# Optimization experiments

Measured on AMD Instinct MI355X. Metric: run time of the kernel, lower is better.

Reference implementation:

```python
import jax, jax.numpy as jnp
import numpy as np


def setup_inputs() -> dict:
    key = jax.random.key(0)
    k0, k1, k2 = jax.random.split(key, 3)
    B, S, H, D = 2, 2048, 16, 128  # flash-attn layout [batch, seq, heads, head_dim]
    q = jax.random.normal(k0, (B, S, H, D), dtype=jnp.float32)
    k = jax.random.normal(k1, (B, S, H, D), dtype=jnp.float32)
    v = jax.random.normal(k2, (B, S, H, D), dtype=jnp.float32)
    return {"_in0": q, "_in1": k, "_in2": v}


def reference(_in0, _in1, _in2):
    # Ring attention computes exact (non-causal, default) scaled dot-product
    # attention over the full sequence; the ring KV rotation is a distributed
    # execution detail, not a change in math. Single-device math:
    q, k, v = _in0, _in1, _in2
    D = q.shape[-1]
    scale = 1.0 / jnp.sqrt(jnp.asarray(D, dtype=q.dtype))
    # scores: [B, H, Sq, Sk]
    scores = jnp.einsum("bqhd,bkhd->bhqk", q, k) * scale
    probs = jax.nn.softmax(scores, axis=-1)
    out = jnp.einsum("bhqk,bkhd->bqhd", probs, v)
    return out
```

## Files before the change

### kernel.cpp

```cpp
#include <hip/hip_runtime.h>
#include <hip/hip_bf16.h>

typedef __attribute__((ext_vector_type(8))) short short8;
typedef __attribute__((ext_vector_type(16))) float f32x16;
typedef __attribute__((ext_vector_type(4))) unsigned int uint4v;

#define NB 2
#define NS 2048
#define NH 16
#define ND 128
#define ROWS (NH * ND)
#define KVBLK 64
#define QBLK 128
#define NTILE (NS / KVBLK)
#define NQB (NS / QBLK)

__device__ __forceinline__ unsigned short f2bf(float f) {
  union { __hip_bfloat16 b; unsigned short u; } c;
  c.b = __float2bfloat16(f);
  return c.u;
}

__device__ __forceinline__ short8 pack8(float4 a, float4 b, float s) {
  short8 r;
  r[0] = (short)f2bf(a.x * s); r[1] = (short)f2bf(a.y * s);
  r[2] = (short)f2bf(a.z * s); r[3] = (short)f2bf(a.w * s);
  r[4] = (short)f2bf(b.x * s); r[5] = (short)f2bf(b.y * s);
  r[6] = (short)f2bf(b.z * s); r[7] = (short)f2bf(b.w * s);
  return r;
}

__device__ __forceinline__ void dma16(const void* g, void* l) {
  __builtin_amdgcn_global_load_lds(
      (const __attribute__((address_space(1))) unsigned int*)g,
      (__attribute__((address_space(3))) unsigned int*)l, 16, 0, 0);
}

__device__ __forceinline__ void pl32swap(unsigned int& a, unsigned int& b) {
  asm("v_permlane32_swap_b32 %0, %1" : "+v"(a), "+v"(b));
}

__global__ __launch_bounds__(256) void prepass_kv(
    const float* __restrict__ Kg, const float* __restrict__ Vg,
    unsigned short* __restrict__ Kb, unsigned short* __restrict__ Vt) {
  const int blk = blockIdx.x;
  const int t = blk & (NTILE - 1);
  const int bh = blk >> 5;
  const int h = bh & (NH - 1);
  const int b = bh >> 4;
  const int tid = threadIdx.x;

  const size_t ibase = (size_t)b * NS * ROWS + (size_t)h * ND + (size_t)t * KVBLK * ROWS;
  const float* Kp = Kg + ibase;
  const float* Vp = Vg + ibase;
  unsigned short* Kbp = Kb + ((size_t)bh * NS + t * KVBLK) * ND;
  unsigned short* Vtp = Vt + (size_t)bh * ND * NS + t * KVBLK;

#pragma unroll
  for (int j = 0; j < 4; ++j) {
    const int r = j * 16 + (tid >> 4);
    const int c0 = (tid & 15) * 8;
    float4 a = *reinterpret_cast<const float4*>(Kp + (size_t)r * ROWS + c0);
    float4 c = *reinterpret_cast<const float4*>(Kp + (size_t)r * ROWS + c0 + 4);
    *reinterpret_cast<short8*>(Kbp + r * ND + c0) = pack8(a, c, 1.0f);
  }

  __shared__ float vt[64][129];
#pragma unroll
  for (int j = 0; j < 4; ++j) {
    const int r = j * 16 + (tid >> 4);
    const int c0 = (tid & 15) * 8;
    float4 a = *reinterpret_cast<const float4*>(Vp + (size_t)r * ROWS + c0);
    float4 c = *reinterpret_cast<const float4*>(Vp + (size_t)r * ROWS + c0 + 4);
    vt[r][c0 + 0] = a.x; vt[r][c0 + 1] = a.y; vt[r][c0 + 2] = a.z; vt[r][c0 + 3] = a.w;
    vt[r][c0 + 4] = c.x; vt[r][c0 + 5] = c.y; vt[r][c0 + 6] = c.z; vt[r][c0 + 7] = c.w;
  }
  __syncthreads();
#pragma unroll
  for (int dj = 0; dj < 4; ++dj) {
    const int d = dj * 32 + (tid >> 3);
    const int s0 = (tid & 7) * 8;
    short8 o8;
#pragma unroll
    for (int k = 0; k < 8; ++k) o8[k] = (short)f2bf(vt[s0 + k][d]);
    *reinterpret_cast<short8*>(Vtp + (size_t)d * NS + s0) = o8;
  }
}

__global__ __launch_bounds__(256, 2) void fattn_fwd(
    const float* __restrict__ Qg, const unsigned short* __restrict__ Kb,
    const unsigned short* __restrict__ Vt, float* __restrict__ Og) {
  __shared__ __align__(16) char lds[65536];
  const int tid = threadIdx.x;
  const int l = tid & 63;
  const int w = tid >> 6;
  const int l31 = l & 31;
  const int hi2 = l >> 5;

  const int orig = blockIdx.x;
  const int wg = (orig & 7) * 64 + (orig >> 3);
  const int qblk = wg & (NQB - 1);
  const int bh = wg >> 4;
  const int h = bh & (NH - 1);
  const int b = bh >> 4;

  const float* Qp = Qg + (size_t)b * NS * ROWS + (size_t)h * ND;
  float* Op = Og + (size_t)b * NS * ROWS + (size_t)h * ND;
  const char* Kbh = (const char*)(Kb + (size_t)bh * NS * ND);
  const char* Vth = (const char*)(Vt + (size_t)bh * ND * NS);

  const float scale = 0.08838834764831845f * 1.4426950408889634f;

  const int qrow = qblk * QBLK + w * 32 + l31;
  short8 qf[8];
  {
    const float* qr = Qp + (size_t)qrow * ROWS + hi2 * 8;
#pragma unroll
    for (int ks = 0; ks < 8; ++ks) {
      float4 a = *reinterpret_cast<const float4*>(qr + ks * 16);
      float4 c = *reinterpret_cast<const float4*>(qr + ks * 16 + 4);
      qf[ks] = pack8(a, c, scale);
    }
  }

  auto stage = [&](int t, char* kd, char* vd) {
    const char* Kt = Kbh + (size_t)t * KVBLK * 256;
#pragma unroll
    for (int i = 0; i < 4; ++i) {
      const int instr = w * 4 + i;
      const int row = instr * 4 + (l >> 4);
      const int x = (l & 15) << 4;
      dma16(Kt + row * 256 + (x ^ ((row & 7) << 4)), kd + instr * 1024);
    }
    const char* Vtt = Vth + (size_t)t * KVBLK * 2;
#pragma unroll
    for (int j = 0; j < 4; ++j) {
      const int instr = w * 4 + j;
      const int d = instr * 8 + (l >> 3);
      const int x = (l & 7) << 4;
      dma16(Vtt + (size_t)d * (NS * 2) + (x ^ ((d & 7) << 4)), vd + instr * 1024);
    }
  };

  f32x16 o[4];
#pragma unroll
  for (int dt = 0; dt < 4; ++dt) o[dt] = 0.f;
  float l_acc = 0.f;

  stage(0, lds, lds + 16384);
  asm volatile("s_waitcnt vmcnt(0)" ::: "memory");
  __syncthreads();

#pragma unroll 1
  for (int t = 0; t < NTILE; ++t) {
    char* ksb = lds + (t & 1) * 32768;
    char* vtb = ksb + 16384;
    if (t + 1 < NTILE) {
      char* kn = lds + ((t + 1) & 1) * 32768;
      stage(t + 1, kn, kn + 16384);
    }

    f32x16 st[2];
    __builtin_amdgcn_s_setprio(1);
#pragma unroll
    for (int mt = 0; mt < 2; ++mt) {
      f32x16 acc = 0.f;
      const int row = mt * 32 + l31;
#pragma unroll
      for (int ks = 0; ks < 8; ++ks) {
        short8 kf = *reinterpret_cast<const short8*>(
            ksb + row * 256 + ((ks * 32 + hi2 * 16) ^ ((row & 7) << 4)));
        acc = __builtin_amdgcn_mfma_f32_32x32x16_bf16(kf, qf[ks], acc, 0, 0, 0);
      }
      st[mt] = acc;
    }
    __builtin_amdgcn_s_setprio(0);

    f32x16 p0, p1;
#pragma unroll
    for (int r = 0; r < 16; ++r) p0[r] = exp2f(st[0][r]);
#pragma unroll
    for (int r = 0; r < 16; ++r) p1[r] = exp2f(st[1][r]);
    {
      float s = 0.f;
#pragma unroll
      for (int r = 0; r < 16; ++r) s += p0[r] + p1[r];
      l_acc += s;
    }

    short8 pf[4];
#pragma unroll
    for (int mt = 0; mt < 2; ++mt) {
      const f32x16& pp = mt ? p1 : p0;
      unsigned int X[8];
#pragma unroll
      for (int j = 0; j < 8; ++j)
        X[j] = (unsigned int)f2bf(pp[2 * j]) | ((unsigned int)f2bf(pp[2 * j + 1]) << 16);
      pl32swap(X[0], X[2]); pl32swap(X[1], X[3]);
      pl32swap(X[4], X[6]); pl32swap(X[5], X[7]);
      uint4v lo_ = {X[0], X[1], X[2], X[3]};
      uint4v hi_ = {X[4], X[5], X[6], X[7]};
      pf[mt * 2 + 0] = __builtin_bit_cast(short8, lo_);
      pf[mt * 2 + 1] = __builtin_bit_cast(short8, hi_);
    }

    __builtin_amdgcn_s_setprio(1);
#pragma unroll
    for (int dt = 0; dt < 4; ++dt) {
      const int d = dt * 32 + l31;
#pragma unroll
      for (int ks = 0; ks < 4; ++ks) {
        short8 vf = *reinterpret_cast<const short8*>(
            vtb + d * 128 + ((ks * 32 + hi2 * 16) ^ ((d & 7) << 4)));
        o[dt] = __builtin_amdgcn_mfma_f32_32x32x16_bf16(vf, pf[ks], o[dt], 0, 0, 0);
      }
    }
    __builtin_amdgcn_s_setprio(0);

    if (t + 1 < NTILE) {
      asm volatile("s_waitcnt vmcnt(0)" ::: "memory");
      __syncthreads();
    }
  }

  const float lt = l_acc + __shfl_xor(l_acc, 32);
  const float inv = 1.0f / lt;
  float* orow = Op + (size_t)qrow * ROWS;
#pragma unroll
  for (int dt = 0; dt < 4; ++dt) {
#pragma unroll
    for (int g = 0; g < 4; ++g) {
      float4 v;
      v.x = o[dt][g * 4 + 0] * inv;
      v.y = o[dt][g * 4 + 1] * inv;
      v.z = o[dt][g * 4 + 2] * inv;
      v.w = o[dt][g * 4 + 3] * inv;
      *reinterpret_cast<float4*>(orow + dt * 32 + g * 8 + hi2 * 4) = v;
    }
  }
}

extern "C" void kernel_launch(void* const* d_in, const int* in_sizes, int n_in,
                              void* d_out, int out_size, void* d_ws, size_t ws_size,
                              hipStream_t stream) {
  const float* q = (const float*)d_in[0];
  const float* k = (const float*)d_in[1];
  const float* v = (const float*)d_in[2];
  float* out = (float*)d_out;
  (void)in_sizes; (void)n_in; (void)out_size; (void)ws_size;
  const size_t elems = (size_t)NB * NH * NS * ND;
  unsigned short* Kb = (unsigned short*)d_ws;
  unsigned short* Vt = Kb + elems;
  prepass_kv<<<dim3(NB * NH * NTILE), dim3(256), 0, stream>>>(k, v, Kb, Vt);
  const int nblocks = NQB * NB * NH;
  fattn_fwd<<<dim3(nblocks), dim3(256), 0, stream>>>(q, Kb, Vt, out);
}
```

Before: 113.4 us.

## Pre-swizzle K/V into contiguous LDS-ready tiles and interleave softmax per subtile

The prepass now writes K and transposed V as contiguous 16KB tiles already XOR-swizzled (16-way) in the exact LDS layout. The attention kernel's DMA staging becomes a flat, fully contiguous copy instead of strided row gathers. The V tile stores two d-rows per 256B row with a 16-row swizzle to reduce LDS bank conflicts. It also computes exp/pack per 32-row score subtile right after its MFMAs, which lowers register pressure and allows overlap. This adds index math in the V reads and changes the workspace layout.

```diff
diff --git a/kernel.cpp b/kernel.cpp
--- a/kernel.cpp
+++ b/kernel.cpp
@@ -14,6 +14,7 @@
 #define QBLK 128
 #define NTILE (NS / KVBLK)
 #define NQB (NS / QBLK)
+#define TILEB 16384
 
 __device__ __forceinline__ unsigned short f2bf(float f) {
   union { __hip_bfloat16 b; unsigned short u; } c;
@@ -42,7 +43,7 @@
 
 __global__ __launch_bounds__(256) void prepass_kv(
     const float* __restrict__ Kg, const float* __restrict__ Vg,
-    unsigned short* __restrict__ Kb, unsigned short* __restrict__ Vt) {
+    char* __restrict__ Kbt, char* __restrict__ Vbt) {
   const int blk = blockIdx.x;
   const int t = blk & (NTILE - 1);
   const int bh = blk >> 5;
@@ -53,16 +54,17 @@
   const size_t ibase = (size_t)b * NS * ROWS + (size_t)h * ND + (size_t)t * KVBLK * ROWS;
   const float* Kp = Kg + ibase;
   const float* Vp = Vg + ibase;
-  unsigned short* Kbp = Kb + ((size_t)bh * NS + t * KVBLK) * ND;
-  unsigned short* Vtp = Vt + (size_t)bh * ND * NS + t * KVBLK;
+  char* Kt = Kbt + (size_t)blk * TILEB;
+  char* Vt = Vbt + (size_t)blk * TILEB;
 
 #pragma unroll
   for (int j = 0; j < 4; ++j) {
     const int r = j * 16 + (tid >> 4);
-    const int c0 = (tid & 15) * 8;
-    float4 a = *reinterpret_cast<const float4*>(Kp + (size_t)r * ROWS + c0);
-    float4 c = *reinterpret_cast<const float4*>(Kp + (size_t)r * ROWS + c0 + 4);
-    *reinterpret_cast<short8*>(Kbp + r * ND + c0) = pack8(a, c, 1.0f);
+    const int c = tid & 15;
+    const float* src = Kp + (size_t)r * ROWS + c * 8;
+    float4 a = *reinterpret_cast<const float4*>(src);
+    float4 d = *reinterpret_cast<const float4*>(src + 4);
+    *reinterpret_cast<short8*>(Kt + r * 256 + (((c ^ (r & 15)) << 4))) = pack8(a, d, 1.0f);
   }
 
   __shared__ float vt[64][129];
@@ -71,25 +73,28 @@
     const int r = j * 16 + (tid >> 4);
     const int c0 = (tid & 15) * 8;
     float4 a = *reinterpret_cast<const float4*>(Vp + (size_t)r * ROWS + c0);
-    float4 c = *reinterpret_cast<const float4*>(Vp + (size_t)r * ROWS + c0 + 4);
+    float4 d = *reinterpret_cast<const float4*>(Vp + (size_t)r * ROWS + c0 + 4);
     vt[r][c0 + 0] = a.x; vt[r][c0 + 1] = a.y; vt[r][c0 + 2] = a.z; vt[r][c0 + 3] = a.w;
-    vt[r][c0 + 4] = c.x; vt[r][c0 + 5] = c.y; vt[r][c0 + 6] = c.z; vt[r][c0 + 7] = c.w;
+    vt[r][c0 + 4] = d.x; vt[r][c0 + 5] = d.y; vt[r][c0 + 6] = d.z; vt[r][c0 + 7] = d.w;
   }
   __syncthreads();
 #pragma unroll
-  for (int dj = 0; dj < 4; ++dj) {
-    const int d = dj * 32 + (tid >> 3);
-    const int s0 = (tid & 7) * 8;
+  for (int it = 0; it < 4; ++it) {
+    const int item = it * 256 + tid;
+    const int r = item >> 4;
+    const int j = item & 15;
+    const int d = 2 * r + (j >> 3);
+    const int k0 = (j & 7) * 8;
     short8 o8;
 #pragma unroll
-    for (int k = 0; k < 8; ++k) o8[k] = (short)f2bf(vt[s0 + k][d]);
-    *reinterpret_cast<short8*>(Vtp + (size_t)d * NS + s0) = o8;
+    for (int i = 0; i < 8; ++i) o8[i] = (short)f2bf(vt[k0 + i][d]);
+    *reinterpret_cast<short8*>(Vt + r * 256 + (((j ^ (r & 15)) << 4))) = o8;
   }
 }
 
 __global__ __launch_bounds__(256, 2) void fattn_fwd(
-    const float* __restrict__ Qg, const unsigned short* __restrict__ Kb,
-    const unsigned short* __restrict__ Vt, float* __restrict__ Og) {
+    const float* __restrict__ Qg, const char* __restrict__ Kbt,
+    const char* __restrict__ Vbt, float* __restrict__ Og) {
   __shared__ __align__(16) char lds[65536];
   const int tid = threadIdx.x;
   const int l = tid & 63;
@@ -106,8 +111,8 @@
 
   const float* Qp = Qg + (size_t)b * NS * ROWS + (size_t)h * ND;
   float* Op = Og + (size_t)b * NS * ROWS + (size_t)h * ND;
-  const char* Kbh = (const char*)(Kb + (size_t)bh * NS * ND);
-  const char* Vth = (const char*)(Vt + (size_t)bh * ND * NS);
+  const char* Ktiles = Kbt + (size_t)bh * NTILE * TILEB;
+  const char* Vtiles = Vbt + (size_t)bh * NTILE * TILEB;
 
   const float scale = 0.08838834764831845f * 1.4426950408889634f;
 
@@ -124,21 +129,17 @@
   }
 
   auto stage = [&](int t, char* kd, char* vd) {
-    const char* Kt = Kbh + (size_t)t * KVBLK * 256;
+    const char* Ksrc = Ktiles + (size_t)t * TILEB;
+    const char* Vsrc = Vtiles + (size_t)t * TILEB;
 #pragma unroll
     for (int i = 0; i < 4; ++i) {
       const int instr = w * 4 + i;
-      const int row = instr * 4 + (l >> 4);
-      const int x = (l & 15) << 4;
-      dma16(Kt + row * 256 + (x ^ ((row & 7) << 4)), kd + instr * 1024);
-    }
-    const char* Vtt = Vth + (size_t)t * KVBLK * 2;
-#pragma unroll
-    for (int j = 0; j < 4; ++j) {
-      const int instr = w * 4 + j;
-      const int d = instr * 8 + (l >> 3);
-      const int x = (l & 7) << 4;
-      dma16(Vtt + (size_t)d * (NS * 2) + (x ^ ((d & 7) << 4)), vd + instr * 1024);
+      dma16(Ksrc + instr * 1024 + l * 16, kd + instr * 1024);
+    }
+#pragma unroll
+    for (int i = 0; i < 4; ++i) {
+      const int instr = w * 4 + i;
+      dma16(Vsrc + instr * 1024 + l * 16, vd + instr * 1024);
     }
   };
 
@@ -160,58 +161,54 @@
       stage(t + 1, kn, kn + 16384);
     }
 
-    f32x16 st[2];
-    __builtin_amdgcn_s_setprio(1);
+    short8 pf[4];
 #pragma unroll
     for (int mt = 0; mt < 2; ++mt) {
       f32x16 acc = 0.f;
       const int row = mt * 32 + l31;
+      const int rsw = (row & 15) << 4;
+      __builtin_amdgcn_s_setprio(1);
 #pragma unroll
       for (int ks = 0; ks < 8; ++ks) {
         short8 kf = *reinterpret_cast<const short8*>(
-            ksb + row * 256 + ((ks * 32 + hi2 * 16) ^ ((row & 7) << 4)));
+            ksb + row * 256 + ((ks * 32 + hi2 * 16) ^ rsw));
         acc = __builtin_amdgcn_mfma_f32_32x32x16_bf16(kf, qf[ks], acc, 0, 0, 0);
       }
-      st[mt] = acc;
-    }
-    __builtin_amdgcn_s_setprio(0);
-
-    f32x16 p0, p1;
-#pragma unroll
-    for (int r = 0; r < 16; ++r) p0[r] = exp2f(st[0][r]);
-#pragma unroll
-    for (int r = 0; r < 16; ++r) p1[r] = exp2f(st[1][r]);
-    {
-      float s = 0.f;
-#pragma unroll
-      for (int r = 0; r < 16; ++r) s += p0[r] + p1[r];
-      l_acc += s;
-    }
-
-    short8 pf[4];
-#pragma unroll
-    for (int mt = 0; mt < 2; ++mt) {
-      const f32x16& pp = mt ? p1 : p0;
-      unsigned int X[8];
-#pragma unroll
-      for (int j = 0; j < 8; ++j)
-        X[j] = (unsigned int)f2bf(pp[2 * j]) | ((unsigned int)f2bf(pp[2 * j + 1]) << 16);
-      pl32swap(X[0], X[2]); pl32swap(X[1], X[3]);
-      pl32swap(X[4], X[6]); pl32swap(X[5], X[7]);
-      uint4v lo_ = {X[0], X[1], X[2], X[3]};
-      uint4v hi_ = {X[4], X[5], X[6], X[7]};
-      pf[mt * 2 + 0] = __builtin_bit_cast(short8, lo_);
-      pf[mt * 2 + 1] = __builtin_bit_cast(short8, hi_);
+      __builtin_amdgcn_s_setprio(0);
+      f32x16 p;
+#pragma unroll
+      for (int r = 0; r < 16; ++r) p[r] = exp2f(acc[r]);
+      {
+        float s = 0.f;
+#pragma unroll
+        for (int r = 0; r < 16; ++r) s += p[r];
+        l_acc += s;
+      }
+#pragma unroll
+      for (int half = 0; half < 2; ++half) {
+        unsigned int X[4];
+#pragma unroll
+        for (int j = 0; j < 4; ++j)
+          X[j] = (unsigned int)f2bf(p[half * 8 + 2 * j]) |
+                 ((unsigned int)f2bf(p[half * 8 + 2 * j + 1]) << 16);
+        pl32swap(X[0], X[2]);
+        pl32swap(X[1], X[3]);
+        uint4v u = {X[0], X[1], X[2], X[3]};
+        pf[mt * 2 + half] = __builtin_bit_cast(short8, u);
+      }
     }
 
     __builtin_amdgcn_s_setprio(1);
 #pragma unroll
     for (int dt = 0; dt < 4; ++dt) {
       const int d = dt * 32 + l31;
+      const int vrow = d >> 1;
+      const int vsw = (vrow & 15) << 4;
+      const int doff = (d & 1) * 128;
 #pragma unroll
       for (int ks = 0; ks < 4; ++ks) {
         short8 vf = *reinterpret_cast<const short8*>(
-            vtb + d * 128 + ((ks * 32 + hi2 * 16) ^ ((d & 7) << 4)));
+            vtb + vrow * 256 + ((doff + ks * 32 + hi2 * 16) ^ vsw));
         o[dt] = __builtin_amdgcn_mfma_f32_32x32x16_bf16(vf, pf[ks], o[dt], 0, 0, 0);
       }
     }
@@ -248,10 +245,8 @@
   const float* v = (const float*)d_in[2];
   float* out = (float*)d_out;
   (void)in_sizes; (void)n_in; (void)out_size; (void)ws_size;
-  const size_t elems = (size_t)NB * NH * NS * ND;
-  unsigned short* Kb = (unsigned short*)d_ws;
-  unsigned short* Vt = Kb + elems;
-  prepass_kv<<<dim3(NB * NH * NTILE), dim3(256), 0, stream>>>(k, v, Kb, Vt);
-  const int nblocks = NQB * NB * NH;
-  fattn_fwd<<<dim3(nblocks), dim3(256), 0, stream>>>(q, Kb, Vt, out);
-}
+  char* Kbt = (char*)d_ws;
+  char* Vbt = Kbt + (size_t)NB * NH * NTILE * TILEB;
+  prepass_kv<<<dim3(NB * NH * NTILE), dim3(256), 0, stream>>>(k, v, Kbt, Vbt);
+  fattn_fwd<<<dim3(NQB * NB * NH), dim3(256), 0, stream>>>(q, Kbt, Vbt, out);
+}
```

Result: faster. 110.5 us (-2.5%).
